# Optimization experiments

Hardware: AMD Instinct MI355X
Metric: run time of the kernel (lower is better)

## Reference

```python
import jax, jax.numpy as jnp
import numpy as np
from jax import lax

D = 64          # n_concepts
NT = 16         # n_tasks
H = 256         # prior_units
HID = 256       # prior_hids[0]
K = 3           # n_components
B = 4096
IN = 3 * D + NT + 1  # GRU input size


def setup_inputs() -> dict:
    key = jax.random.key(0)
    ks = jax.random.split(key, 12)
    s = 0.05
    z = jax.random.normal(ks[0], (B, D), jnp.float32)
    c = jax.random.normal(ks[1], (B, D + NT), jnp.float32)
    b = jnp.round(jax.random.uniform(ks[2], (B, D), jnp.float32))
    m = jnp.round(jax.random.uniform(ks[3], (B, D), jnp.float32))
    # GRU cell params (torch layout: [3H, in], gates r,z,n)
    gru_w_ih = jax.random.normal(ks[4], (3 * H, IN), jnp.float32) * s
    gru_w_hh = jax.random.normal(ks[5], (3 * H, H), jnp.float32) * s
    gru_b_ih = jax.random.normal(ks[6], (3 * H,), jnp.float32) * s
    gru_b_hh = jax.random.normal(ks[7], (3 * H,), jnp.float32) * s
    # MLP head: Linear(H+3D+NT -> HID), Tanh, Linear(HID -> 3K)
    w1 = jax.random.normal(ks[8], (HID, H + 3 * D + NT), jnp.float32) * s
    b1 = jax.random.normal(ks[9], (HID,), jnp.float32) * s
    w2 = jax.random.normal(ks[10], (3 * K, HID), jnp.float32) * s
    b2 = jax.random.normal(ks[11], (3 * K,), jnp.float32) * s
    return dict(z=z, c=c, b=b, m=m, gru_w_ih=gru_w_ih, gru_w_hh=gru_w_hh,
                gru_b_ih=gru_b_ih, gru_b_hh=gru_b_hh, w1=w1, b1=b1, w2=w2, b2=b2)


def _logp(z, c, b, m, gru_w_ih, gru_w_hh, gru_b_ih, gru_b_hh, w1, b1, w2, b2):
    Bn, d = z.shape
    cbm = jnp.concatenate([c, b, m], axis=1)             # [B, 3D+NT]
    # z_prev per step: -1 at t=0, then z[:, t-1]
    z_prev = jnp.concatenate([-jnp.ones((Bn, 1), z.dtype), z[:, :-1]], axis=1)  # [B, D]
    # input projection: only the first input column (z_t) varies per step
    const_ih = cbm @ gru_w_ih[:, 1:].T + gru_b_ih        # [B, 3H]
    w_ih_z = gru_w_ih[:, 0]                              # [3H]

    def gru_step(h, zp):
        gi = zp[:, None] * w_ih_z[None, :] + const_ih    # [B, 3H]
        gh = h @ gru_w_hh.T + gru_b_hh                   # [B, 3H]
        i_r, i_z, i_n = jnp.split(gi, 3, axis=1)
        h_r, h_z, h_n = jnp.split(gh, 3, axis=1)
        r = jax.nn.sigmoid(i_r + h_r)
        zg = jax.nn.sigmoid(i_z + h_z)
        n = jnp.tanh(i_n + r * h_n)
        h_new = (1.0 - zg) * n + zg * h
        return h_new, h_new

    h0 = jnp.zeros((Bn, H), z.dtype)
    _, hs = lax.scan(gru_step, h0, z_prev.T)             # hs: [D, B, H]

    # MLP head applied to [h_t, c, b, m] for every step at once
    cbm_rep = jnp.broadcast_to(cbm[None], (d,) + cbm.shape)
    mlp_in = jnp.concatenate([hs, cbm_rep], axis=2)      # [D, B, H+3D+NT]
    h1 = jnp.tanh(mlp_in @ w1.T + b1)
    params = (h1 @ w2.T + b2).transpose(1, 0, 2)         # [B, D, 3K]

    logits = params[..., :K]
    means = params[..., K:2 * K]
    lsigmas = params[..., 2 * K:]
    targets = z[..., None]                               # [B, D, 1]
    log_norm = -lsigmas - 0.5 * np.log(2.0 * np.pi).astype(np.float32)
    log_kernel = -0.5 * jnp.square((targets - means) * jnp.exp(-lsigmas))
    log_like = (jax.nn.logsumexp(log_kernel + log_norm + logits, axis=-1)
                - jax.nn.logsumexp(logits, axis=-1))     # [B, D]

    query = m * (1.0 - b)
    mask = jnp.flip(jnp.sort(query, axis=1), axis=1)     # descending sorted values
    return jnp.sum(log_like * mask, axis=1)              # [B]


def reference(z, c, b, m, gru_w_ih, gru_w_hh, gru_b_ih, gru_b_hh, w1, b1, w2, b2):
    return _logp(z, c, b, m, gru_w_ih, gru_w_hh, gru_b_ih, gru_b_hh, w1, b1, w2, b2)
```

## Files before the change

### kernel.cpp

```cpp
#include <hip/hip_runtime.h>

typedef __attribute__((ext_vector_type(8))) short short8;
typedef __attribute__((ext_vector_type(4))) float floatx4;

#define LOG2E     1.4426950408889634f
#define TWO_LOG2E 2.8853900817779268f

__device__ __forceinline__ unsigned short f2bf(float x) {
  union { float f; unsigned u; } v; v.f = x;
  unsigned r = v.u + 0x7fffu + ((v.u >> 16) & 1u);
  return (unsigned short)(r >> 16);
}
__device__ __forceinline__ float sigm_fast(float s) {
  return __builtin_amdgcn_rcpf(1.f + __builtin_amdgcn_exp2f(-s));
}
__device__ __forceinline__ float tanh_fast(float y) {
  return fmaf(-2.f, __builtin_amdgcn_rcpf(1.f + __builtin_amdgcn_exp2f(y)), 1.f);
}
__device__ __forceinline__ floatx4 splat4(float v) { floatx4 r; r[0]=v; r[1]=v; r[2]=v; r[3]=v; return r; }

#define N_WHH  (768*256)
#define N_WCAT (1024*256)
#define N_W1H  (256*256)
#define N_W2   (16*256)
#define N_TOT  (N_WHH + N_WCAT + N_W1H + N_W2)

#define GROW(r) (((((r)&7) ^ ((((r)>>3)&1)*5))) << 4)
#define A_SW(kk,q,row) ((((kk)<<6)+((q)<<4)) ^ GROW(row))

__global__ void prep_kernel(const float* __restrict__ w_hh, const float* __restrict__ w_ih,
                            const float* __restrict__ w1,  const float* __restrict__ w2,
                            unsigned short* __restrict__ Whh, unsigned short* __restrict__ Wcat,
                            unsigned short* __restrict__ W1h, unsigned short* __restrict__ W2b) {
  int i = blockIdx.x * blockDim.x + threadIdx.x;
  if (i < N_WHH) {
    int n = i >> 8;
    Whh[i] = f2bf(w_hh[i] * (n < 512 ? LOG2E : TWO_LOG2E));
  } else if (i < N_WHH + N_WCAT) {
    int j = i - N_WHH; int n = j >> 8, k = j & 255;
    float v = 0.f;
    if (k < 208) {
      if (n < 768) v = w_ih[n * 209 + 1 + k] * (n < 512 ? LOG2E : TWO_LOG2E);
      else         v = w1[(n - 768) * 464 + 256 + k] * TWO_LOG2E;
    }
    Wcat[j] = f2bf(v);
  } else if (i < N_WHH + N_WCAT + N_W1H) {
    int j = i - N_WHH - N_WCAT; int n = j >> 8, k = j & 255;
    W1h[j] = f2bf(w1[n * 464 + k] * TWO_LOG2E);
  } else if (i < N_TOT) {
    int j = i - N_WHH - N_WCAT - N_W1H; int n = j >> 8, k = j & 255;
    W2b[j] = (n < 9) ? f2bf(w2[n * 256 + k]) : (unsigned short)0;
  }
}

__launch_bounds__(512, 1)
__global__ void const_kernel(const float* __restrict__ cc, const float* __restrict__ bb,
                             const float* __restrict__ mmat,
                             const float* __restrict__ b_ih, const float* __restrict__ b_hh,
                             const float* __restrict__ b1,
                             const unsigned short* __restrict__ Wcat,
                             float* __restrict__ CST, float* __restrict__ cnt,
                             float* __restrict__ cntmax) {
  __shared__ __align__(16) char smem[8192];
  const int tid = threadIdx.x;
  const int w = tid >> 6, l = tid & 63, q = l >> 4, li = l & 15;
  const int r0 = blockIdx.x << 4;

  {
    int row = tid >> 5, ch = tid & 31;
    float v[8];
#pragma unroll
    for (int j = 0; j < 8; j++) v[j] = 0.f;
    if (ch < 10) {
      const float* s = cc + (size_t)(r0 + row) * 80 + ch * 8;
#pragma unroll
      for (int j = 0; j < 8; j++) v[j] = s[j];
    } else if (ch < 18) {
      const float* s = bb + (size_t)(r0 + row) * 64 + (ch - 10) * 8;
#pragma unroll
      for (int j = 0; j < 8; j++) v[j] = s[j];
    } else if (ch < 26) {
      const float* s = mmat + (size_t)(r0 + row) * 64 + (ch - 18) * 8;
#pragma unroll
      for (int j = 0; j < 8; j++) v[j] = s[j];
    }
    short8 pk;
#pragma unroll
    for (int j = 0; j < 8; j++) pk[j] = (short)f2bf(v[j]);
    *(short8*)(smem + row * 512 + ((ch * 16) ^ GROW(row))) = pk;
  }
  __syncthreads();

  int col[8];
  floatx4 acc[8];
#pragma unroll
  for (int tt = 0; tt < 8; tt++) {
    col[tt] = (w * 8 + tt) * 16 + li;
    float bv;
    if (col[tt] < 512)      bv = LOG2E * (b_ih[col[tt]] + b_hh[col[tt]]);
    else if (col[tt] < 768) bv = TWO_LOG2E * b_ih[col[tt]];
    else                    bv = TWO_LOG2E * b1[col[tt] - 768];
    acc[tt] = splat4(bv);
  }
#pragma unroll
  for (int kk = 0; kk < 7; kk++) {
    short8 a = *(const short8*)(smem + li * 512 + A_SW(kk, q, li));
#pragma unroll
    for (int tt = 0; tt < 8; tt++) {
      short8 bf = *(const short8*)(Wcat + (size_t)col[tt] * 256 + kk * 32 + q * 8);
      acc[tt] = __builtin_amdgcn_mfma_f32_16x16x32_bf16(a, bf, acc[tt], 0, 0, 0);
    }
  }
#pragma unroll
  for (int tt = 0; tt < 8; tt++)
#pragma unroll
    for (int r = 0; r < 4; r++)
      CST[(size_t)(r0 + q * 4 + r) * 1024 + col[tt]] = acc[tt][r];

  if (w == 0 && l < 16) {
    const float* bp = bb + (size_t)(r0 + l) * 64;
    const float* mp = mmat + (size_t)(r0 + l) * 64;
    float s = 0.f;
#pragma unroll 8
    for (int k2 = 0; k2 < 64; k2++) s += mp[k2] * (1.f - bp[k2]);
    cnt[r0 + l] = s;
    float mx = s;
#pragma unroll
    for (int off = 8; off; off >>= 1) mx = fmaxf(mx, __shfl_xor(mx, off, 16));
    if (l == 0) cntmax[blockIdx.x] = mx;
  }
}

__launch_bounds__(512, 1)
__global__ void gru_kernel(const float* __restrict__ z, const float* __restrict__ w_ih,
                           const float* __restrict__ b_hh,
                           const unsigned short* __restrict__ Whh,
                           const float* __restrict__ CST,
                           const float* __restrict__ cntmax,
                           char* __restrict__ hs) {
  __shared__ __align__(16) char smem[151552];
  const int tid = threadIdx.x;
  const int w = tid >> 6, l = tid & 63, q = l >> 4, li = l & 15;
  const int r0 = blockIdx.x << 4;
  const int nsteps = (int)(cntmax[blockIdx.x] + 0.5f);

#pragma unroll
  for (int c = tid; c < 8192; c += 512) {
    int i = c >> 5, j = c & 31;
    short8 v = *(const short8*)(Whh + (size_t)(512 + i) * 256 + j * 8);
    *(short8*)(smem + i * 512 + ((j * 16) ^ GROW(i))) = v;
  }
  *(floatx4*)(smem + 131072 + tid * 16) = splat4(0.f);
  {
    float* zb = (float*)(smem + 147456);
    int i0 = tid;
    zb[i0] = z[(size_t)(r0 + (i0 & 15)) * 64 + (i0 >> 4)];
    int i1 = tid + 512;
    zb[i1] = z[(size_t)(r0 + (i1 & 15)) * 64 + (i1 >> 4)];
  }

  int ncol6[6];
#pragma unroll
  for (int tt = 0; tt < 6; tt++) ncol6[tt] = (tt >> 1) * 256 + (w << 5) + ((tt & 1) << 4) + li;

  short8 wreg[4][8];
#pragma unroll
  for (int u4 = 0; u4 < 4; u4++)
#pragma unroll
    for (int kk = 0; kk < 8; kk++)
      wreg[u4][kk] = *(const short8*)(Whh + (size_t)ncol6[u4] * 256 + kk * 32 + q * 8);

  floatx4 cst[6];
#pragma unroll
  for (int tt = 0; tt < 6; tt++)
#pragma unroll
    for (int r = 0; r < 4; r++)
      cst[tt][r] = CST[(size_t)(r0 + q * 4 + r) * 1024 + ncol6[tt]];

  float wz[6];
#pragma unroll
  for (int tt = 0; tt < 6; tt++)
    wz[tt] = w_ih[(size_t)ncol6[tt] * 209] * (tt < 4 ? LOG2E : TWO_LOG2E);
  float bhhn[2];
#pragma unroll
  for (int nc = 0; nc < 2; nc++) bhhn[nc] = b_hh[ncol6[4 + nc]] * TWO_LOG2E;

  float hreg[8];
#pragma unroll
  for (int j = 0; j < 8; j++) hreg[j] = 0.f;

  __syncthreads();
  char* hs_blk = hs + (size_t)blockIdx.x * 524288;

#pragma unroll 1
  for (int t = 0; t < nsteps; t++) {
    const char* hp = smem + 131072 + (t & 1) * 8192;
    char* hc = smem + 131072 + ((t + 1) & 1) * 8192;

    floatx4 acc[6];
#pragma unroll
    for (int u4 = 0; u4 < 4; u4++) acc[u4] = splat4(0.f);
#pragma unroll
    for (int nc = 0; nc < 2; nc++) acc[4 + nc] = splat4(bhhn[nc]);

#pragma unroll
    for (int kk = 0; kk < 8; kk++) {
      short8 a = *(const short8*)(hp + li * 512 + A_SW(kk, q, li));
      acc[0] = __builtin_amdgcn_mfma_f32_16x16x32_bf16(a, wreg[0][kk], acc[0], 0, 0, 0);
      acc[1] = __builtin_amdgcn_mfma_f32_16x16x32_bf16(a, wreg[1][kk], acc[1], 0, 0, 0);
      acc[2] = __builtin_amdgcn_mfma_f32_16x16x32_bf16(a, wreg[2][kk], acc[2], 0, 0, 0);
      acc[3] = __builtin_amdgcn_mfma_f32_16x16x32_bf16(a, wreg[3][kk], acc[3], 0, 0, 0);
#pragma unroll
      for (int nc = 0; nc < 2; nc++) {
        int i = (w << 5) + (nc << 4) + li;
        short8 bn = *(const short8*)(smem + i * 512 + A_SW(kk, q, i));
        acc[4 + nc] = __builtin_amdgcn_mfma_f32_16x16x32_bf16(a, bn, acc[4 + nc], 0, 0, 0);
      }
    }

    floatx4 zpv;
    if (t == 0) zpv = splat4(-1.f);
    else        zpv = *(const floatx4*)(smem + 147456 + (t - 1) * 64 + (q << 4));

#pragma unroll
    for (int nc = 0; nc < 2; nc++) {
#pragma unroll
      for (int r = 0; r < 4; r++) {
        float rr = sigm_fast(fmaf(zpv[r], wz[nc],     cst[nc][r])     + acc[nc][r]);
        float zg = sigm_fast(fmaf(zpv[r], wz[2 + nc], cst[2 + nc][r]) + acc[2 + nc][r]);
        float nn = tanh_fast(fmaf(rr, acc[4 + nc][r],
                                  fmaf(zpv[r], wz[4 + nc], cst[4 + nc][r])));
        float hv = fmaf(zg, hreg[nc * 4 + r] - nn, nn);
        hreg[nc * 4 + r] = hv;
        int rw = (q << 2) + r;
        int colb = ((w << 5) + (nc << 4) + li) << 1;
        *(unsigned short*)(hc + rw * 512 + (colb ^ GROW(rw))) = f2bf(hv);
      }
    }
    __syncthreads();
    *(short8*)(hs_blk + (size_t)t * 8192 + tid * 16) = *(const short8*)(hc + tid * 16);
  }
}

__launch_bounds__(512, 2)
__global__ void mlp_kernel(const float* __restrict__ z, const float* __restrict__ b2,
                           const float* __restrict__ cnt, const float* __restrict__ cntmax,
                           const unsigned short* __restrict__ W1h,
                           const unsigned short* __restrict__ W2b,
                           const float* __restrict__ CST, const char* __restrict__ hs,
                           float* __restrict__ part) {
  __shared__ __align__(16) char smem[35968];
  const int tid = threadIdx.x;
  const int w = tid >> 6, l = tid & 63, q = l >> 4, li = l & 15;
  const int tg = blockIdx.x >> 8, rg = blockIdx.x & 255;
  const int r0 = rg << 4;

  const int nsteps = (int)(cntmax[rg] + 0.5f);
  const int count = (nsteps - tg + 1) >> 1;
  if (count <= 0) {
    if (tid < 16) part[rg * 32 + tg * 16 + tid] = 0.f;
    return;
  }
  const char* img = hs + (size_t)rg * 524288;

  {
    int s = tid >> 4, row = tid & 15;
    ((float*)(smem + 33920))[tid] = z[(size_t)(r0 + row) * 64 + tg + 2 * s];
  }

  int col[2];
#pragma unroll
  for (int nc = 0; nc < 2; nc++) col[nc] = (w << 5) + (nc << 4) + li;

  short8 w1reg[2][8];
#pragma unroll
  for (int nc = 0; nc < 2; nc++)
#pragma unroll
    for (int kk = 0; kk < 8; kk++)
      w1reg[nc][kk] = *(const short8*)(W1h + (size_t)col[nc] * 256 + kk * 32 + q * 8);

  float cst1[2][4];
#pragma unroll
  for (int nc = 0; nc < 2; nc++)
#pragma unroll
    for (int r = 0; r < 4; r++)
      cst1[nc][r] = CST[(size_t)(r0 + q * 4 + r) * 1024 + 768 + col[nc]];

  float b2v = (li < 9) ? b2[li] : 0.f;
  float cl = (l < 16) ? cnt[r0 + l] : 0.f;
  float lacc = 0.f;

  {
    short8 v = *(const short8*)(img + (size_t)tg * 8192 + tid * 16);
    *(short8*)(smem + tid * 16) = v;
  }
  __syncthreads();

#pragma unroll 1
  for (int s = 0; s < count; s++) {
    int t = tg + 2 * s;
    short8 pf;
    bool do_pf = (s + 1 < count);
    if (do_pf) pf = *(const short8*)(img + (size_t)(t + 2) * 8192 + tid * 16);

    floatx4 acc[2];
    acc[0] = splat4(0.f); acc[1] = splat4(0.f);
    const char* As = smem + (s & 1) * 8192;
#pragma unroll
    for (int kk = 0; kk < 8; kk++) {
      short8 a = *(const short8*)(As + li * 512 + A_SW(kk, q, li));
      acc[0] = __builtin_amdgcn_mfma_f32_16x16x32_bf16(a, w1reg[0][kk], acc[0], 0, 0, 0);
      acc[1] = __builtin_amdgcn_mfma_f32_16x16x32_bf16(a, w1reg[1][kk], acc[1], 0, 0, 0);
    }
    char* Us = smem + 16384 + (s & 1) * 8192;
#pragma unroll
    for (int nc = 0; nc < 2; nc++)
#pragma unroll
      for (int r = 0; r < 4; r++) {
        float uv = tanh_fast(acc[nc][r] + cst1[nc][r]);
        int rw = (q << 2) + r;
        int colb = col[nc] << 1;
        *(unsigned short*)(Us + rw * 512 + (colb ^ GROW(rw))) = f2bf(uv);
      }
    if (do_pf) *(short8*)(smem + ((s + 1) & 1) * 8192 + tid * 16) = pf;
    __syncthreads();

    if (w == (s & 7)) {
      floatx4 pacc = splat4(b2v);
#pragma unroll
      for (int kk = 0; kk < 8; kk++) {
        short8 au = *(const short8*)(Us + li * 512 + A_SW(kk, q, li));
        short8 bw = *(const short8*)(W2b + (size_t)li * 256 + kk * 32 + q * 8);
        pacc = __builtin_amdgcn_mfma_f32_16x16x32_bf16(au, bw, pacc, 0, 0, 0);
      }
      float* Pw = (float*)(smem + 32768);
#pragma unroll
      for (int r = 0; r < 4; r++) Pw[((q << 2) + r) * 17 + li] = pacc[r];
      if (l < 16) {
        const float* pr = Pw + l * 17;
        float zt = ((const float*)(smem + 33920))[s * 16 + l];
        float aj[3], lg[3];
#pragma unroll
        for (int j = 0; j < 3; j++) {
          float lgt = pr[j];
          float mean = pr[3 + j];
          float ls = pr[6 + j];
          float d = (zt - mean) * __expf(-ls);
          lg[j] = lgt;
          aj[j] = lgt - ls - 0.9189385332f - 0.5f * d * d;
        }
        float mx = fmaxf(aj[0], fmaxf(aj[1], aj[2]));
        float ln_n = mx + __logf(__expf(aj[0] - mx) + __expf(aj[1] - mx) + __expf(aj[2] - mx));
        float mg = fmaxf(lg[0], fmaxf(lg[1], lg[2]));
        float ln_d = mg + __logf(__expf(lg[0] - mg) + __expf(lg[1] - mg) + __expf(lg[2] - mg));
        if ((float)t + 0.5f < cl) lacc += (ln_n - ln_d);
      }
    }
  }

  __syncthreads();
  if (l < 16) ((float*)(smem + 32768))[w * 16 + l] = lacc;
  __syncthreads();
  if (w == 0 && l < 16) {
    const float* F = (const float*)(smem + 32768);
    float s = 0.f;
#pragma unroll
    for (int ww = 0; ww < 8; ww++) s += F[ww * 16 + l];
    part[rg * 32 + tg * 16 + l] = s;
  }
}

__global__ void reduce_kernel(const float* __restrict__ part, float* __restrict__ out) {
  int i = blockIdx.x * 256 + threadIdx.x;
  if (i < 4096) {
    int rg = i >> 4, row = i & 15;
    const float* p = part + rg * 32 + row;
    out[i] = p[0] + p[16];
  }
}

extern "C" void kernel_launch(void* const* d_in, const int* in_sizes, int n_in,
                              void* d_out, int out_size, void* d_ws, size_t ws_size,
                              hipStream_t stream) {
  const float* z    = (const float*)d_in[0];
  const float* c    = (const float*)d_in[1];
  const float* b    = (const float*)d_in[2];
  const float* m    = (const float*)d_in[3];
  const float* w_ih = (const float*)d_in[4];
  const float* w_hh = (const float*)d_in[5];
  const float* b_ih = (const float*)d_in[6];
  const float* b_hh = (const float*)d_in[7];
  const float* w1   = (const float*)d_in[8];
  const float* b1   = (const float*)d_in[9];
  const float* w2   = (const float*)d_in[10];
  const float* b2   = (const float*)d_in[11];

  char* ws = (char*)d_ws;
  unsigned short* Whh  = (unsigned short*)(ws);
  unsigned short* Wcat = (unsigned short*)(ws + 393216);
  unsigned short* W1h  = (unsigned short*)(ws + 917504);
  unsigned short* W2b  = (unsigned short*)(ws + 1048576);
  float*          CST  = (float*)(ws + 1056768);
  float*          cnt  = (float*)(ws + 17833984);
  float*          cmax = (float*)(ws + 17850368);
  float*          part = (float*)(ws + 17851392);
  char*           hs   = ws + 17916928;

  hipLaunchKernelGGL(prep_kernel, dim3(N_TOT / 256), dim3(256), 0, stream,
                     w_hh, w_ih, w1, w2, Whh, Wcat, W1h, W2b);
  hipLaunchKernelGGL(const_kernel, dim3(256), dim3(512), 0, stream,
                     c, b, m, b_ih, b_hh, b1, Wcat, CST, cnt, cmax);
  hipLaunchKernelGGL(gru_kernel, dim3(256), dim3(512), 0, stream,
                     z, w_ih, b_hh, Whh, CST, cmax, hs);
  hipLaunchKernelGGL(mlp_kernel, dim3(512), dim3(512), 0, stream,
                     z, b2, cnt, cmax, W1h, W2b, CST, hs, part);
  hipLaunchKernelGGL(reduce_kernel, dim3(16), dim3(256), 0, stream,
                     part, (float*)d_out);
}
```

Measured before the change: 206.7 us.

## Restructure GRU recurrence to swap MFMA operands, shrink LDS, split MLP over four step groups

Result: slower. 313.5 us (+51.6%).

```diff
diff --git a/kernel.cpp b/kernel.cpp
--- a/kernel.cpp
+++ b/kernel.cpp
@@ -11,6 +11,13 @@
   unsigned r = v.u + 0x7fffu + ((v.u >> 16) & 1u);
   return (unsigned short)(r >> 16);
 }
+__device__ __forceinline__ unsigned cvt_pk(float lo, float hi) {
+  unsigned r;
+  asm("v_cvt_pk_bf16_f32 %0, %1, %2" : "=v"(r) : "v"(lo), "v"(hi));
+  return r;
+}
+__device__ __forceinline__ float bfp_lo(unsigned p) { return __builtin_bit_cast(float, p << 16); }
+__device__ __forceinline__ float bfp_hi(unsigned p) { return __builtin_bit_cast(float, p & 0xffff0000u); }
 __device__ __forceinline__ float sigm_fast(float s) {
   return __builtin_amdgcn_rcpf(1.f + __builtin_amdgcn_exp2f(-s));
 }
@@ -28,10 +35,13 @@
 #define GROW(r) (((((r)&7) ^ ((((r)>>3)&1)*5))) << 4)
 #define A_SW(kk,q,row) ((((kk)<<6)+((q)<<4)) ^ GROW(row))
 
+#define MF __builtin_amdgcn_mfma_f32_16x16x32_bf16
+
 __global__ void prep_kernel(const float* __restrict__ w_hh, const float* __restrict__ w_ih,
                             const float* __restrict__ w1,  const float* __restrict__ w2,
                             unsigned short* __restrict__ Whh, unsigned short* __restrict__ Wcat,
-                            unsigned short* __restrict__ W1h, unsigned short* __restrict__ W2b) {
+                            unsigned short* __restrict__ W1h, unsigned short* __restrict__ W2b,
+                            float* __restrict__ wzc) {
   int i = blockIdx.x * blockDim.x + threadIdx.x;
   if (i < N_WHH) {
     int n = i >> 8;
@@ -50,6 +60,9 @@
   } else if (i < N_TOT) {
     int j = i - N_WHH - N_WCAT - N_W1H; int n = j >> 8, k = j & 255;
     W2b[j] = (n < 9) ? f2bf(w2[n * 256 + k]) : (unsigned short)0;
+  } else if (i < N_TOT + 768) {
+    int j = i - N_TOT;
+    wzc[j] = w_ih[(size_t)j * 209] * (j < 512 ? LOG2E : TWO_LOG2E);
   }
 }
 
@@ -108,7 +121,7 @@
 #pragma unroll
     for (int tt = 0; tt < 8; tt++) {
       short8 bf = *(const short8*)(Wcat + (size_t)col[tt] * 256 + kk * 32 + q * 8);
-      acc[tt] = __builtin_amdgcn_mfma_f32_16x16x32_bf16(a, bf, acc[tt], 0, 0, 0);
+      acc[tt] = MF(a, bf, acc[tt], 0, 0, 0);
     }
   }
 #pragma unroll
@@ -131,112 +144,141 @@
   }
 }
 
-__launch_bounds__(512, 1)
-__global__ void gru_kernel(const float* __restrict__ z, const float* __restrict__ w_ih,
-                           const float* __restrict__ b_hh,
+__launch_bounds__(512, 2)
+__global__ void gru_kernel(const float* __restrict__ z, const float* __restrict__ b_hh,
                            const unsigned short* __restrict__ Whh,
+                           const float* __restrict__ wzc,
                            const float* __restrict__ CST,
                            const float* __restrict__ cntmax,
                            char* __restrict__ hs) {
-  __shared__ __align__(16) char smem[151552];
+  __shared__ __align__(16) char smem[20480];
   const int tid = threadIdx.x;
   const int w = tid >> 6, l = tid & 63, q = l >> 4, li = l & 15;
   const int r0 = blockIdx.x << 4;
   const int nsteps = (int)(cntmax[blockIdx.x] + 0.5f);
 
-#pragma unroll
-  for (int c = tid; c < 8192; c += 512) {
-    int i = c >> 5, j = c & 31;
-    short8 v = *(const short8*)(Whh + (size_t)(512 + i) * 256 + j * 8);
-    *(short8*)(smem + i * 512 + ((j * 16) ^ GROW(i))) = v;
-  }
-  *(floatx4*)(smem + 131072 + tid * 16) = splat4(0.f);
+  *(floatx4*)(smem + tid * 16) = splat4(0.f);
   {
-    float* zb = (float*)(smem + 147456);
-    int i0 = tid;
-    zb[i0] = z[(size_t)(r0 + (i0 & 15)) * 64 + (i0 >> 4)];
+    float* zb = (float*)(smem + 16384);
+    zb[tid] = z[(size_t)(r0 + (tid & 15)) * 64 + (tid >> 4)];
     int i1 = tid + 512;
     zb[i1] = z[(size_t)(r0 + (i1 & 15)) * 64 + (i1 >> 4)];
   }
 
-  int ncol6[6];
-#pragma unroll
-  for (int tt = 0; tt < 6; tt++) ncol6[tt] = (tt >> 1) * 256 + (w << 5) + ((tt & 1) << 4) + li;
-
-  short8 wreg[4][8];
-#pragma unroll
-  for (int u4 = 0; u4 < 4; u4++)
-#pragma unroll
-    for (int kk = 0; kk < 8; kk++)
-      wreg[u4][kk] = *(const short8*)(Whh + (size_t)ncol6[u4] * 256 + kk * 32 + q * 8);
-
-  floatx4 cst[6];
-#pragma unroll
-  for (int tt = 0; tt < 6; tt++)
-#pragma unroll
-    for (int r = 0; r < 4; r++)
-      cst[tt][r] = CST[(size_t)(r0 + q * 4 + r) * 1024 + ncol6[tt]];
-
-  float wz[6];
-#pragma unroll
-  for (int tt = 0; tt < 6; tt++)
-    wz[tt] = w_ih[(size_t)ncol6[tt] * 209] * (tt < 4 ? LOG2E : TWO_LOG2E);
-  float bhhn[2];
-#pragma unroll
-  for (int nc = 0; nc < 2; nc++) bhhn[nc] = b_hh[ncol6[4 + nc]] * TWO_LOG2E;
-
-  float hreg[8];
-#pragma unroll
-  for (int j = 0; j < 8; j++) hreg[j] = 0.f;
+  short8 wa0[8], wa1[8], wa2[8], wa4[8], wa5[8];
+  {
+    const unsigned short* p0 = Whh + (size_t)((w << 5) + li) * 256 + q * 8;
+    const unsigned short* p1 = Whh + (size_t)((w << 5) + 16 + li) * 256 + q * 8;
+    const unsigned short* p2 = Whh + (size_t)(256 + (w << 5) + li) * 256 + q * 8;
+    const unsigned short* p4 = Whh + (size_t)(512 + (w << 5) + li) * 256 + q * 8;
+    const unsigned short* p5 = Whh + (size_t)(512 + (w << 5) + 16 + li) * 256 + q * 8;
+#pragma unroll
+    for (int kk = 0; kk < 8; kk++) {
+      wa0[kk] = *(const short8*)(p0 + kk * 32);
+      wa1[kk] = *(const short8*)(p1 + kk * 32);
+      wa2[kk] = *(const short8*)(p2 + kk * 32);
+      wa4[kk] = *(const short8*)(p4 + kk * 32);
+      wa5[kk] = *(const short8*)(p5 + kk * 32);
+    }
+  }
+
+  const size_t crow = (size_t)(r0 + li) * 1024;
+  unsigned crz[4][2], cn[2][2], bh[2][2], wz[6][2];
+#pragma unroll
+  for (int tt = 0; tt < 4; tt++) {
+    int base = (tt >> 1) * 256 + (w << 5) + ((tt & 1) << 4) + (q << 2);
+    floatx4 c = *(const floatx4*)(CST + crow + base);
+    crz[tt][0] = cvt_pk(c[0], c[1]); crz[tt][1] = cvt_pk(c[2], c[3]);
+  }
+#pragma unroll
+  for (int nc = 0; nc < 2; nc++) {
+    int base = 512 + (w << 5) + (nc << 4) + (q << 2);
+    floatx4 c = *(const floatx4*)(CST + crow + base);
+    cn[nc][0] = cvt_pk(c[0], c[1]); cn[nc][1] = cvt_pk(c[2], c[3]);
+    floatx4 b = *(const floatx4*)(b_hh + base);
+    bh[nc][0] = cvt_pk(b[0] * TWO_LOG2E, b[1] * TWO_LOG2E);
+    bh[nc][1] = cvt_pk(b[2] * TWO_LOG2E, b[3] * TWO_LOG2E);
+  }
+#pragma unroll
+  for (int tt = 0; tt < 6; tt++) {
+    int base = (tt >> 1) * 256 + (w << 5) + ((tt & 1) << 4) + (q << 2);
+    floatx4 c = *(const floatx4*)(wzc + base);
+    wz[tt][0] = cvt_pk(c[0], c[1]); wz[tt][1] = cvt_pk(c[2], c[3]);
+  }
+
+  unsigned hpk[2][2] = {{0u, 0u}, {0u, 0u}};
 
   __syncthreads();
   char* hs_blk = hs + (size_t)blockIdx.x * 524288;
 
 #pragma unroll 1
   for (int t = 0; t < nsteps; t++) {
-    const char* hp = smem + 131072 + (t & 1) * 8192;
-    char* hc = smem + 131072 + ((t + 1) & 1) * 8192;
-
-    floatx4 acc[6];
-#pragma unroll
-    for (int u4 = 0; u4 < 4; u4++) acc[u4] = splat4(0.f);
-#pragma unroll
-    for (int nc = 0; nc < 2; nc++) acc[4 + nc] = splat4(bhhn[nc]);
-
-#pragma unroll
-    for (int kk = 0; kk < 8; kk++) {
-      short8 a = *(const short8*)(hp + li * 512 + A_SW(kk, q, li));
-      acc[0] = __builtin_amdgcn_mfma_f32_16x16x32_bf16(a, wreg[0][kk], acc[0], 0, 0, 0);
-      acc[1] = __builtin_amdgcn_mfma_f32_16x16x32_bf16(a, wreg[1][kk], acc[1], 0, 0, 0);
-      acc[2] = __builtin_amdgcn_mfma_f32_16x16x32_bf16(a, wreg[2][kk], acc[2], 0, 0, 0);
-      acc[3] = __builtin_amdgcn_mfma_f32_16x16x32_bf16(a, wreg[3][kk], acc[3], 0, 0, 0);
-#pragma unroll
-      for (int nc = 0; nc < 2; nc++) {
-        int i = (w << 5) + (nc << 4) + li;
-        short8 bn = *(const short8*)(smem + i * 512 + A_SW(kk, q, i));
-        acc[4 + nc] = __builtin_amdgcn_mfma_f32_16x16x32_bf16(a, bn, acc[4 + nc], 0, 0, 0);
-      }
-    }
-
-    floatx4 zpv;
-    if (t == 0) zpv = splat4(-1.f);
-    else        zpv = *(const floatx4*)(smem + 147456 + (t - 1) * 64 + (q << 4));
-
-#pragma unroll
-    for (int nc = 0; nc < 2; nc++) {
-#pragma unroll
-      for (int r = 0; r < 4; r++) {
-        float rr = sigm_fast(fmaf(zpv[r], wz[nc],     cst[nc][r])     + acc[nc][r]);
-        float zg = sigm_fast(fmaf(zpv[r], wz[2 + nc], cst[2 + nc][r]) + acc[2 + nc][r]);
-        float nn = tanh_fast(fmaf(rr, acc[4 + nc][r],
-                                  fmaf(zpv[r], wz[4 + nc], cst[4 + nc][r])));
-        float hv = fmaf(zg, hreg[nc * 4 + r] - nn, nn);
-        hreg[nc * 4 + r] = hv;
-        int rw = (q << 2) + r;
-        int colb = ((w << 5) + (nc << 4) + li) << 1;
-        *(unsigned short*)(hc + rw * 512 + (colb ^ GROW(rw))) = f2bf(hv);
-      }
-    }
+    const char* hp = smem + ((t & 1) << 13);
+    char* hc = smem + (((t + 1) & 1) << 13);
+
+    const unsigned short* w3p = Whh + (size_t)(256 + (w << 5) + 16 + li) * 256 + q * 8;
+    asm("" : "+v"(w3p));
+
+    floatx4 a0, a1, a2, a3, a4, a5;
+    a0[0]=bfp_lo(crz[0][0]); a0[1]=bfp_hi(crz[0][0]); a0[2]=bfp_lo(crz[0][1]); a0[3]=bfp_hi(crz[0][1]);
+    a1[0]=bfp_lo(crz[1][0]); a1[1]=bfp_hi(crz[1][0]); a1[2]=bfp_lo(crz[1][1]); a1[3]=bfp_hi(crz[1][1]);
+    a2[0]=bfp_lo(crz[2][0]); a2[1]=bfp_hi(crz[2][0]); a2[2]=bfp_lo(crz[2][1]); a2[3]=bfp_hi(crz[2][1]);
+    a3[0]=bfp_lo(crz[3][0]); a3[1]=bfp_hi(crz[3][0]); a3[2]=bfp_lo(crz[3][1]); a3[3]=bfp_hi(crz[3][1]);
+    a4 = splat4(0.f); a5 = splat4(0.f);
+
+#define LDH(kk) (*(const short8*)(hp + li * 512 + A_SW(kk, q, li)))
+    short8 bA = LDH(0), bB = LDH(1);
+    short8 w3A = *(const short8*)(w3p);
+    short8 w3B = *(const short8*)(w3p + 32);
+
+#define KSTEP(kk, bX, w3X, bY, w3Y)                                         \
+    a0 = MF(wa0[kk], bX, a0, 0, 0, 0);                                      \
+    a1 = MF(wa1[kk], bX, a1, 0, 0, 0);                                      \
+    a2 = MF(wa2[kk], bX, a2, 0, 0, 0);                                      \
+    a3 = MF(w3X,     bX, a3, 0, 0, 0);                                      \
+    a4 = MF(wa4[kk], bX, a4, 0, 0, 0);                                      \
+    a5 = MF(wa5[kk], bX, a5, 0, 0, 0);                                      \
+    if ((kk) < 6) { bX = LDH((kk) + 2); w3X = *(const short8*)(w3p + ((kk) + 2) * 32); }
+
+    KSTEP(0, bA, w3A, bB, w3B)
+    KSTEP(1, bB, w3B, bA, w3A)
+    KSTEP(2, bA, w3A, bB, w3B)
+    KSTEP(3, bB, w3B, bA, w3A)
+    KSTEP(4, bA, w3A, bB, w3B)
+    KSTEP(5, bB, w3B, bA, w3A)
+    KSTEP(6, bA, w3A, bB, w3B)
+    KSTEP(7, bB, w3B, bA, w3A)
+#undef KSTEP
+#undef LDH
+
+    float zp = -1.f;
+    if (t) zp = ((const float*)(smem + 16384))[(t - 1) * 16 + li];
+
+#define GATE(nc, pr, aR, aZ, aN)                                                    \
+    {                                                                               \
+      float rlo = sigm_fast(fmaf(zp, bfp_lo(wz[0 + nc][pr]), aR[2 * pr]));          \
+      float rhi = sigm_fast(fmaf(zp, bfp_hi(wz[0 + nc][pr]), aR[2 * pr + 1]));      \
+      float zlo = sigm_fast(fmaf(zp, bfp_lo(wz[2 + nc][pr]), aZ[2 * pr]));          \
+      float zhi = sigm_fast(fmaf(zp, bfp_hi(wz[2 + nc][pr]), aZ[2 * pr + 1]));      \
+      float gnlo = fmaf(zp, bfp_lo(wz[4 + nc][pr]), bfp_lo(cn[nc][pr]));            \
+      float gnhi = fmaf(zp, bfp_hi(wz[4 + nc][pr]), bfp_hi(cn[nc][pr]));            \
+      float nlo = tanh_fast(fmaf(rlo, aN[2 * pr] + bfp_lo(bh[nc][pr]), gnlo));      \
+      float nhi = tanh_fast(fmaf(rhi, aN[2 * pr + 1] + bfp_hi(bh[nc][pr]), gnhi));  \
+      unsigned hop = hpk[nc][pr];                                                   \
+      float hlo = fmaf(zlo, bfp_lo(hop) - nlo, nlo);                                \
+      float hhi = fmaf(zhi, bfp_hi(hop) - nhi, nhi);                                \
+      unsigned np = cvt_pk(hlo, hhi);                                               \
+      hpk[nc][pr] = np;                                                             \
+      *(unsigned*)(hc + li * 512 +                                                  \
+        (((w << 6) + ((nc) << 5) + (q << 3) + ((pr) << 2)) ^ GROW(li))) = np;       \
+    }
+
+    GATE(0, 0, a0, a2, a4)
+    GATE(0, 1, a0, a2, a4)
+    GATE(1, 0, a1, a3, a5)
+    GATE(1, 1, a1, a3, a5)
+#undef GATE
+
     __syncthreads();
     *(short8*)(hs_blk + (size_t)t * 8192 + tid * 16) = *(const short8*)(hc + tid * 16);
   }
@@ -248,24 +290,21 @@
                            const unsigned short* __restrict__ W1h,
                            const unsigned short* __restrict__ W2b,
                            const float* __restrict__ CST, const char* __restrict__ hs,
-                           float* __restrict__ part) {
-  __shared__ __align__(16) char smem[35968];
+                           float* __restrict__ out) {
+  __shared__ __align__(16) char smem[34880];
   const int tid = threadIdx.x;
   const int w = tid >> 6, l = tid & 63, q = l >> 4, li = l & 15;
   const int tg = blockIdx.x >> 8, rg = blockIdx.x & 255;
   const int r0 = rg << 4;
 
   const int nsteps = (int)(cntmax[rg] + 0.5f);
-  const int count = (nsteps - tg + 1) >> 1;
-  if (count <= 0) {
-    if (tid < 16) part[rg * 32 + tg * 16 + tid] = 0.f;
-    return;
-  }
+  const int count = (nsteps - tg + 3) >> 2;
+  if (count <= 0) return;
   const char* img = hs + (size_t)rg * 524288;
 
-  {
+  if (tid < 256) {
     int s = tid >> 4, row = tid & 15;
-    ((float*)(smem + 33920))[tid] = z[(size_t)(r0 + row) * 64 + tg + 2 * s];
+    ((float*)(smem + 33856))[tid] = z[(size_t)(r0 + row) * 64 + tg + 4 * s];
   }
 
   int col[2];
@@ -298,10 +337,10 @@
 
 #pragma unroll 1
   for (int s = 0; s < count; s++) {
-    int t = tg + 2 * s;
+    int t = tg + 4 * s;
     short8 pf;
     bool do_pf = (s + 1 < count);
-    if (do_pf) pf = *(const short8*)(img + (size_t)(t + 2) * 8192 + tid * 16);
+    if (do_pf) pf = *(const short8*)(img + (size_t)(t + 4) * 8192 + tid * 16);
 
     floatx4 acc[2];
     acc[0] = splat4(0.f); acc[1] = splat4(0.f);
@@ -309,8 +348,8 @@
 #pragma unroll
     for (int kk = 0; kk < 8; kk++) {
       short8 a = *(const short8*)(As + li * 512 + A_SW(kk, q, li));
-      acc[0] = __builtin_amdgcn_mfma_f32_16x16x32_bf16(a, w1reg[0][kk], acc[0], 0, 0, 0);
-      acc[1] = __builtin_amdgcn_mfma_f32_16x16x32_bf16(a, w1reg[1][kk], acc[1], 0, 0, 0);
+      acc[0] = MF(a, w1reg[0][kk], acc[0], 0, 0, 0);
+      acc[1] = MF(a, w1reg[1][kk], acc[1], 0, 0, 0);
     }
     char* Us = smem + 16384 + (s & 1) * 8192;
 #pragma unroll
@@ -331,14 +370,14 @@
       for (int kk = 0; kk < 8; kk++) {
         short8 au = *(const short8*)(Us + li * 512 + A_SW(kk, q, li));
         short8 bw = *(const short8*)(W2b + (size_t)li * 256 + kk * 32 + q * 8);
-        pacc = __builtin_amdgcn_mfma_f32_16x16x32_bf16(au, bw, pacc, 0, 0, 0);
+        pacc = MF(au, bw, pacc, 0, 0, 0);
       }
       float* Pw = (float*)(smem + 32768);
 #pragma unroll
       for (int r = 0; r < 4; r++) Pw[((q << 2) + r) * 17 + li] = pacc[r];
       if (l < 16) {
         const float* pr = Pw + l * 17;
-        float zt = ((const float*)(smem + 33920))[s * 16 + l];
+        float zt = ((const float*)(smem + 33856))[s * 16 + l];
         float aj[3], lg[3];
 #pragma unroll
         for (int j = 0; j < 3; j++) {
@@ -366,16 +405,7 @@
     float s = 0.f;
 #pragma unroll
     for (int ww = 0; ww < 8; ww++) s += F[ww * 16 + l];
-    part[rg * 32 + tg * 16 + l] = s;
-  }
-}
-
-__global__ void reduce_kernel(const float* __restrict__ part, float* __restrict__ out) {
-  int i = blockIdx.x * 256 + threadIdx.x;
-  if (i < 4096) {
-    int rg = i >> 4, row = i & 15;
-    const float* p = part + rg * 32 + row;
-    out[i] = p[0] + p[16];
+    atomicAdd(&out[r0 + l], s);
   }
 }
 
@@ -403,17 +433,16 @@
   float*          CST  = (float*)(ws + 1056768);
   float*          cnt  = (float*)(ws + 17833984);
   float*          cmax = (float*)(ws + 17850368);
-  float*          part = (float*)(ws + 17851392);
+  float*          wzc  = (float*)(ws + 17851392);
   char*           hs   = ws + 17916928;
 
-  hipLaunchKernelGGL(prep_kernel, dim3(N_TOT / 256), dim3(256), 0, stream,
-                     w_hh, w_ih, w1, w2, Whh, Wcat, W1h, W2b);
+  hipMemsetAsync(d_out, 0, (size_t)out_size * sizeof(float), stream);
+  hipLaunchKernelGGL(prep_kernel, dim3((N_TOT + 768) / 256), dim3(256), 0, stream,
+                     w_hh, w_ih, w1, w2, Whh, Wcat, W1h, W2b, wzc);
   hipLaunchKernelGGL(const_kernel, dim3(256), dim3(512), 0, stream,
                      c, b, m, b_ih, b_hh, b1, Wcat, CST, cnt, cmax);
   hipLaunchKernelGGL(gru_kernel, dim3(256), dim3(512), 0, stream,
-                     z, w_ih, b_hh, Whh, CST, cmax, hs);
-  hipLaunchKernelGGL(mlp_kernel, dim3(512), dim3(512), 0, stream,
-                     z, b2, cnt, cmax, W1h, W2b, CST, hs, part);
-  hipLaunchKernelGGL(reduce_kernel, dim3(16), dim3(256), 0, stream,
-                     part, (float*)d_out);
-}
+                     z, b_hh, Whh, wzc, CST, cmax, hs);
+  hipLaunchKernelGGL(mlp_kernel, dim3(1024), dim3(512), 0, stream,
+                     z, b2, cnt, cmax, W1h, W2b, CST, hs, (float*)d_out);
+}
```
